# Kernel tuning notes

Hardware: AMD Instinct MI355X
Metric: run time of the kernel (lower is better)

The kernel has to match this reference:

```python
import jax, jax.numpy as jnp
import numpy as np

NUM_HEADS = 16

def _stablemax3_s(x):
    # 3rd-order Taylor approx of exp(x), Eq 38
    pos = 1.0 + x * (1.0 + 0.5 * x * (1.0 + x / 3.0))
    neg = 1.0 / (1.0 - x * (1.0 - 0.5 * x * (1.0 - x / 3.0)))
    return jnp.where(x >= 0, pos, neg)

def stablemax3(logits, axis=-1):
    logits = logits - jnp.max(logits, axis=axis, keepdims=True)
    s = _stablemax3_s(logits)
    return s / jnp.sum(s, axis=axis, keepdims=True)

def setup_inputs() -> dict:
    key = jax.random.key(0)
    k1, k2, k3 = jax.random.split(key, 3)
    B, S, D = 2, 2048, 1024
    x = jax.random.normal(k1, (B, S, D), dtype=jnp.float32)
    w_qkv = jax.random.normal(k2, (3 * D, D), dtype=jnp.float32) * 0.02
    w_out = jax.random.normal(k3, (D, D), dtype=jnp.float32) * 0.02
    b_out = jnp.zeros((D,), dtype=jnp.float32)
    return {"x": x, "w_qkv": w_qkv, "w_out": w_out, "b_out": b_out}

def reference(x, w_qkv, w_out, b_out):
    B, S, D = x.shape
    H = NUM_HEADS
    hd = D // H
    scale = hd ** (-0.5)
    qkv = x @ w_qkv.T                                  # [B, S, 3D]
    qkv = qkv.reshape(B, S, 3, H, hd)
    qkv = jnp.transpose(qkv, (2, 0, 3, 1, 4))          # [3, B, H, S, hd]
    q, k, v = qkv[0], qkv[1], qkv[2]                   # pos(.) is identity here
    attn = jnp.einsum('bhsd,bhtd->bhst', q, k) * scale # [B, H, S, S]
    attn = stablemax3(attn, axis=-1)
    out = jnp.einsum('bhst,bhtd->bhsd', attn, v)       # [B, H, S, hd]
    out = jnp.transpose(out, (0, 2, 1, 3)).reshape(B, S, D)
    return out @ w_out.T + b_out
```

## Files before the change

kernel.cpp:

```cpp
#include <hip/hip_runtime.h>

typedef _Float16 half8 __attribute__((ext_vector_type(8)));
typedef _Float16 half4 __attribute__((ext_vector_type(4)));
typedef _Float16 half2v __attribute__((ext_vector_type(2)));
typedef float floatx4 __attribute__((ext_vector_type(4)));
typedef unsigned int uint2v __attribute__((ext_vector_type(2)));
typedef unsigned int uint4v __attribute__((ext_vector_type(4)));

__device__ __forceinline__ void gl_lds16(const _Float16* g, _Float16* l) {
    __builtin_amdgcn_global_load_lds(
        (const __attribute__((address_space(1))) void*)g,
        (__attribute__((address_space(3))) void*)l, 16, 0, 0);
}

__device__ __forceinline__ half2v cvt_pk(float a, float b) {
    return __builtin_bit_cast(half2v, __builtin_amdgcn_cvt_pkrtz(a, b));
}

__device__ __forceinline__ half2v rcp2(half2v d) {
#if __has_builtin(__builtin_amdgcn_rcph)
    half2v r;
    r[0] = __builtin_amdgcn_rcph(d[0]);
    r[1] = __builtin_amdgcn_rcph(d[1]);
    return r;
#else
    half2v r;
    r[0] = (_Float16)__builtin_amdgcn_rcpf((float)d[0]);
    r[1] = (_Float16)__builtin_amdgcn_rcpf((float)d[1]);
    return r;
#endif
}

__device__ __forceinline__ float dot2acc(half2v a, float acc) {
#if __has_builtin(__builtin_amdgcn_fdot2)
    const half2v one = {(_Float16)1.0f, (_Float16)1.0f};
    return __builtin_amdgcn_fdot2(a, one, acc, false);
#else
    return acc + (float)a[0] + (float)a[1];
#endif
}

__device__ __forceinline__ half8 from4(half2v a, half2v b, half2v c, half2v d) {
    uint4v u = {__builtin_bit_cast(unsigned int, a), __builtin_bit_cast(unsigned int, b),
                __builtin_bit_cast(unsigned int, c), __builtin_bit_cast(unsigned int, d)};
    return __builtin_bit_cast(half8, u);
}

__device__ __forceinline__ half8 from_lohi(half4 lo, half4 hi) {
    uint2v l = __builtin_bit_cast(uint2v, lo);
    uint2v h = __builtin_bit_cast(uint2v, hi);
    uint4v u = {l[0], l[1], h[0], h[1]};
    return __builtin_bit_cast(half8, u);
}

__global__ __launch_bounds__(256) void cvt_xw(const floatx4* __restrict__ x,
                                              const floatx4* __restrict__ wq,
                                              half4* __restrict__ xh,
                                              half4* __restrict__ wqh) {
    int i = blockIdx.x * 256 + threadIdx.x;
    floatx4 v;
    half4 h;
    if (i < 1048576) {
        v = x[i];
#pragma unroll
        for (int j = 0; j < 4; ++j) h[j] = (_Float16)v[j];
        xh[i] = h;
    } else {
        int j4 = i - 1048576;
        v = wq[j4];
#pragma unroll
        for (int j = 0; j < 4; ++j) h[j] = (_Float16)v[j];
        wqh[j4] = h;
    }
}

__global__ __launch_bounds__(256) void cvt_f32_f16(const floatx4* __restrict__ in,
                                                   half4* __restrict__ out, int n4) {
    int i = blockIdx.x * 256 + threadIdx.x;
    if (i >= n4) return;
    floatx4 v = in[i];
    half4 h;
#pragma unroll
    for (int j = 0; j < 4; ++j) h[j] = (_Float16)v[j];
    out[i] = h;
}

__global__ __launch_bounds__(256) void gemm_qkv(const _Float16* __restrict__ A,
                                                const _Float16* __restrict__ B,
                                                _Float16* __restrict__ qh,
                                                _Float16* __restrict__ kh,
                                                _Float16* __restrict__ vth) {
    const int K = 1024;
    __shared__ _Float16 SH[128 * 68];
    _Float16* As = SH;
    _Float16* Bs = SH + 4096;
    const int t = threadIdx.x;
    const int lane = t & 63, w = t >> 6;
    const int l15 = lane & 15, quad = lane >> 4;
    const int wm = w >> 1, wn = w & 1;
    const int m0 = blockIdx.y * 128, n0 = blockIdx.x * 128;

    floatx4 acc[4][4];
    const floatx4 zf = {0.f, 0.f, 0.f, 0.f};
#pragma unroll
    for (int i = 0; i < 4; ++i)
#pragma unroll
        for (int j = 0; j < 4; ++j) acc[i][j] = zf;

    for (int kt = 0; kt < K; kt += 32) {
        __syncthreads();
#pragma unroll
        for (int it = 0; it < 2; ++it) {
            int cc = it * 256 + t;
            int row = cc >> 2, kc = cc & 3;
            gl_lds16(&A[(size_t)(m0 + row) * K + kt + kc * 8], &As[cc * 8]);
            gl_lds16(&B[(size_t)(n0 + row) * K + kt + kc * 8], &Bs[cc * 8]);
        }
        __syncthreads();
        half8 af[4], bfr[4];
#pragma unroll
        for (int i = 0; i < 4; ++i)
            af[i] = *(const half8*)&As[(wm * 64 + i * 16 + l15) * 32 + quad * 8];
#pragma unroll
        for (int i = 0; i < 4; ++i)
            bfr[i] = *(const half8*)&Bs[(wn * 64 + i * 16 + l15) * 32 + quad * 8];
#pragma unroll
        for (int mi = 0; mi < 4; ++mi)
#pragma unroll
            for (int ni = 0; ni < 4; ++ni)
                acc[mi][ni] = __builtin_amdgcn_mfma_f32_16x16x32_f16(af[mi], bfr[ni],
                                                                     acc[mi][ni], 0, 0, 0);
    }

    const int b = m0 >> 11, s0 = m0 & 2047;
#pragma unroll
    for (int hf = 0; hf < 2; ++hf) {
        __syncthreads();
        if (wn == hf) {
#pragma unroll
            for (int mi = 0; mi < 4; ++mi)
#pragma unroll
                for (int ni = 0; ni < 4; ++ni)
#pragma unroll
                    for (int r = 0; r < 4; ++r)
                        SH[(wm * 64 + mi * 16 + quad * 4 + r) * 68 + ni * 16 + l15] =
                            (_Float16)acc[mi][ni][r];
        }
        __syncthreads();
        const int cbase = n0 + hf * 64;
        if (n0 < 2048) {
            const int hh = (cbase & 1023) >> 6;
            _Float16* dst = (n0 < 1024 ? qh : kh) + (size_t)((b << 4) | hh) * 131072;
#pragma unroll
            for (int it = 0; it < 4; ++it) {
                int cc = it * 256 + t;
                int r = cc >> 3, c8 = cc & 7;
                half4 lo = *(const half4*)&SH[r * 68 + c8 * 8];
                half4 hi = *(const half4*)&SH[r * 68 + c8 * 8 + 4];
                *(half8*)&dst[(size_t)(s0 + r) * 64 + c8 * 8] = from_lohi(lo, hi);
            }
        } else {
            const int hh = (cbase - 2048) >> 6;
            _Float16* dst = vth + (size_t)((b << 4) | hh) * 131072;
#pragma unroll
            for (int it = 0; it < 4; ++it) {
                int cc = it * 256 + t;
                int d = cc >> 4, s8 = cc & 15;
                int sq = s8 & 7;
                int base = (s8 >> 3) * 64 + (sq >> 2) * 32 + (sq & 3) * 4;
                half8 v;
#pragma unroll
                for (int j = 0; j < 8; ++j)
                    v[j] = SH[(base + (j >> 2) * 16 + (j & 3)) * 68 + d];
                *(half8*)&dst[(size_t)d * 2048 + s0 + s8 * 8] = v;
            }
        }
    }
}

__global__ __launch_bounds__(256) void gemm_out(const _Float16* __restrict__ A,
                                                const _Float16* __restrict__ B,
                                                float* __restrict__ C,
                                                const float* __restrict__ bias) {
    const int K = 1024, N = 1024;
    __shared__ _Float16 SH[6144];
    _Float16* As = SH;
    _Float16* Bs = SH + 2048;
    const int t = threadIdx.x;
    const int lane = t & 63, w = t >> 6;
    const int l15 = lane & 15, quad = lane >> 4;
    const int wm = w >> 1, wn = w & 1;
    const int m0 = blockIdx.y * 64, n0 = blockIdx.x * 128;

    floatx4 acc[2][4];
    const floatx4 zf = {0.f, 0.f, 0.f, 0.f};
#pragma unroll
    for (int i = 0; i < 2; ++i)
#pragma unroll
        for (int j = 0; j < 4; ++j) acc[i][j] = zf;

    for (int kt = 0; kt < K; kt += 32) {
        __syncthreads();
        {
            int row = t >> 2, kc = t & 3;
            gl_lds16(&A[(size_t)(m0 + row) * K + kt + kc * 8], &As[t * 8]);
        }
#pragma unroll
        for (int it = 0; it < 2; ++it) {
            int cc = it * 256 + t;
            int row = cc >> 2, kc = cc & 3;
            gl_lds16(&B[(size_t)(n0 + row) * K + kt + kc * 8], &Bs[cc * 8]);
        }
        __syncthreads();
        half8 af[2], bfr[4];
#pragma unroll
        for (int i = 0; i < 2; ++i)
            af[i] = *(const half8*)&As[(wm * 32 + i * 16 + l15) * 32 + quad * 8];
#pragma unroll
        for (int i = 0; i < 4; ++i)
            bfr[i] = *(const half8*)&Bs[(wn * 64 + i * 16 + l15) * 32 + quad * 8];
#pragma unroll
        for (int mi = 0; mi < 2; ++mi)
#pragma unroll
            for (int ni = 0; ni < 4; ++ni)
                acc[mi][ni] = __builtin_amdgcn_mfma_f32_16x16x32_f16(af[mi], bfr[ni],
                                                                     acc[mi][ni], 0, 0, 0);
    }

#pragma unroll
    for (int mi = 0; mi < 2; ++mi) {
#pragma unroll
        for (int ni = 0; ni < 4; ++ni) {
            int col = n0 + wn * 64 + ni * 16 + l15;
            float bv = bias[col];
#pragma unroll
            for (int r = 0; r < 4; ++r) {
                int row = m0 + wm * 32 + mi * 16 + quad * 4 + r;
                C[(size_t)row * N + col] = acc[mi][ni][r] + bv;
            }
        }
    }
}

__global__ __launch_bounds__(256, 4) void attn_kernel(const _Float16* __restrict__ qh,
                                                      const _Float16* __restrict__ kh,
                                                      const _Float16* __restrict__ vth,
                                                      _Float16* __restrict__ out) {
    __shared__ _Float16 SM[16384];

    const int t = threadIdx.x;
    const int lane = t & 63, w = t >> 6;
    const int l15 = lane & 15, quad = lane >> 4;
    const int sw = l15 & 7;
    const int qg = w >> 1, kg = w & 1;
    const int bh = blockIdx.x;
    const int q0 = blockIdx.y * 64;
    const int b = bh >> 4, h = bh & 15;

    const _Float16* Qp = qh + (size_t)bh * 131072 + q0 * 64;
    const _Float16* Kp = kh + (size_t)bh * 131072;
    const _Float16* VTp = vth + (size_t)bh * 131072;

    const int row0 = t >> 3, cg0 = (t & 7) ^ (row0 & 7);
    const _Float16* K0 = &Kp[(size_t)row0 * 64 + cg0 * 8];
    const _Float16* V0 = &VTp[(size_t)row0 * 2048 + cg0 * 8];

    const floatx4 zf = {0.f, 0.f, 0.f, 0.f};

    half8 qf[2][2];
#pragma unroll
    for (int nh = 0; nh < 2; ++nh)
#pragma unroll
        for (int kk = 0; kk < 2; ++kk) {
            half8 q = *(const half8*)&Qp[(qg * 32 + nh * 16 + l15) * 64 + kk * 32 + quad * 8];
#pragma unroll
            for (int j = 0; j < 8; ++j) q[j] = q[j] * (_Float16)0.125f;
            qf[nh][kk] = q;
        }

    float rmax[2] = {-1.0e30f, -1.0e30f};
#pragma unroll
    for (int s = 0; s < 4; ++s)
        gl_lds16(K0 + s * 2048, &SM[s * 2048 + t * 8]);
    __syncthreads();
    {
        const _Float16* sKp = K0 + 8192;
        for (int i = 0, cur = 0; i < 16; ++i, cur ^= 1) {
            if (i < 15) {
                _Float16* kd = cur ? &SM[0] : &SM[8192];
#pragma unroll
                for (int s = 0; s < 4; ++s)
                    gl_lds16(sKp + s * 2048, kd + s * 2048 + t * 8);
                sKp += 8192;
            }
            const _Float16* Ks = cur ? &SM[8192] : &SM[0];
            half8 kf0[4], kf1[4];
#pragma unroll
            for (int Ti = 0; Ti < 4; ++Ti) {
                const int rb = ((kg * 4 + Ti) * 16 + l15) << 6;
                kf0[Ti] = *(const half8*)&Ks[rb + ((quad ^ sw) << 3)];
                kf1[Ti] = *(const half8*)&Ks[rb + (((4 + quad) ^ sw) << 3)];
            }
            floatx4 sa[4][2];
            __builtin_amdgcn_s_setprio(1);
#pragma unroll
            for (int Ti = 0; Ti < 4; ++Ti)
#pragma unroll
                for (int nh = 0; nh < 2; ++nh)
                    sa[Ti][nh] = __builtin_amdgcn_mfma_f32_16x16x32_f16(kf0[Ti], qf[nh][0],
                                                                        zf, 0, 0, 0);
#pragma unroll
            for (int Ti = 0; Ti < 4; ++Ti)
#pragma unroll
                for (int nh = 0; nh < 2; ++nh)
                    sa[Ti][nh] = __builtin_amdgcn_mfma_f32_16x16x32_f16(kf1[Ti], qf[nh][1],
                                                                        sa[Ti][nh], 0, 0, 0);
            __builtin_amdgcn_s_setprio(0);
#pragma unroll
            for (int Ti = 0; Ti < 4; ++Ti)
#pragma unroll
                for (int nh = 0; nh < 2; ++nh)
#pragma unroll
                    for (int r = 0; r < 4; ++r)
                        rmax[nh] = fmaxf(rmax[nh], sa[Ti][nh][r]);
            __syncthreads();
        }
    }
#pragma unroll
    for (int nh = 0; nh < 2; ++nh) {
        rmax[nh] = fmaxf(rmax[nh], __shfl_xor(rmax[nh], 16, 64));
        rmax[nh] = fmaxf(rmax[nh], __shfl_xor(rmax[nh], 32, 64));
    }
    {
        float* EXM = (float*)SM;
        if (quad == 0) {
#pragma unroll
            for (int nh = 0; nh < 2; ++nh)
                EXM[((qg * 2 + nh) * 2 + kg) * 16 + l15] = rmax[nh];
        }
        __syncthreads();
#pragma unroll
        for (int nh = 0; nh < 2; ++nh)
            rmax[nh] = fmaxf(EXM[((qg * 2 + nh) * 2 + 0) * 16 + l15],
                             EXM[((qg * 2 + nh) * 2 + 1) * 16 + l15]);
        __syncthreads();
    }
    const floatx4 xmv[2] = {{-rmax[0], -rmax[0], -rmax[0], -rmax[0]},
                            {-rmax[1], -rmax[1], -rmax[1], -rmax[1]}};

    const half2v cA = {(_Float16)(-1.0f / 6.0f), (_Float16)(-1.0f / 6.0f)};
    const half2v cB = {(_Float16)0.5f, (_Float16)0.5f};
    const half2v cC = {(_Float16)-1.0f, (_Float16)-1.0f};
    const half2v cD = {(_Float16)1.0f, (_Float16)1.0f};

    float rsum[2] = {0.f, 0.f};
    floatx4 oacc[4][2];
#pragma unroll
    for (int i = 0; i < 4; ++i) { oacc[i][0] = zf; oacc[i][1] = zf; }

    auto tile_step = [&](const _Float16* Ks, const _Float16* VTs) {
        half8 kf0[2], kf1[2];
#pragma unroll
        for (int Ti = 0; Ti < 2; ++Ti) {
            const int rb = ((kg * 2 + Ti) * 16 + l15) << 6;
            kf0[Ti] = *(const half8*)&Ks[rb + ((quad ^ sw) << 3)];
            kf1[Ti] = *(const half8*)&Ks[rb + (((4 + quad) ^ sw) << 3)];
        }
        floatx4 sa[2][2];
        __builtin_amdgcn_s_setprio(1);
#pragma unroll
        for (int Ti = 0; Ti < 2; ++Ti)
#pragma unroll
            for (int nh = 0; nh < 2; ++nh)
                sa[Ti][nh] = __builtin_amdgcn_mfma_f32_16x16x32_f16(kf0[Ti], qf[nh][0],
                                                                    xmv[nh], 0, 0, 0);
#pragma unroll
        for (int Ti = 0; Ti < 2; ++Ti)
#pragma unroll
            for (int nh = 0; nh < 2; ++nh)
                sa[Ti][nh] = __builtin_amdgcn_mfma_f32_16x16x32_f16(kf1[Ti], qf[nh][1],
                                                                    sa[Ti][nh], 0, 0, 0);
        __builtin_amdgcn_s_setprio(0);
        half8 vf[4];
#pragma unroll
        for (int di = 0; di < 4; ++di)
            vf[di] = *(const half8*)&VTs[((di * 16 + l15) << 6) +
                                         ((((kg << 2) + quad) ^ sw) << 3)];
#pragma unroll
        for (int nh = 0; nh < 2; ++nh) {
            half2v p2m[4];
#pragma unroll
            for (int m = 0; m < 4; ++m) {
                int Ti = m >> 1;
                int r0 = (m & 1) * 2;
                half2v x2 = cvt_pk(sa[Ti][nh][r0], sa[Ti][nh][r0 + 1]);
                half2v hp = __builtin_elementwise_fma(x2, cA, cB);
                hp = __builtin_elementwise_fma(x2, hp, cC);
                hp = __builtin_elementwise_fma(x2, hp, cD);
                half2v p2 = rcp2(hp);
                rsum[nh] = dot2acc(p2, rsum[nh]);
                p2m[m] = p2;
            }
            half8 pb = from4(p2m[0], p2m[1], p2m[2], p2m[3]);
            __builtin_amdgcn_s_setprio(1);
#pragma unroll
            for (int di = 0; di < 4; ++di)
                oacc[di][nh] = __builtin_amdgcn_mfma_f32_16x16x32_f16(vf[di], pb,
                                                                      oacc[di][nh], 0, 0, 0);
            __builtin_amdgcn_s_setprio(0);
        }
    };

    gl_lds16(K0, &SM[t * 8]);
    gl_lds16(K0 + 2048, &SM[2048 + t * 8]);
    gl_lds16(V0, &SM[8192 + t * 8]);
    gl_lds16(V0 + 65536, &SM[8192 + 2048 + t * 8]);
    __syncthreads();

    {
        const _Float16* sK = K0 + 4096;
        const _Float16* sV = V0 + 64;
        for (int i = 0; i < 16; ++i) {
            gl_lds16(sK, &SM[4096 + t * 8]);
            gl_lds16(sK + 2048, &SM[4096 + 2048 + t * 8]);
            gl_lds16(sV, &SM[12288 + t * 8]);
            gl_lds16(sV + 65536, &SM[12288 + 2048 + t * 8]);
            sK += 4096; sV += 64;
            tile_step(&SM[0], &SM[8192]);
            __syncthreads();
            if (i < 15) {
                gl_lds16(sK, &SM[t * 8]);
                gl_lds16(sK + 2048, &SM[2048 + t * 8]);
                gl_lds16(sV, &SM[8192 + t * 8]);
                gl_lds16(sV + 65536, &SM[8192 + 2048 + t * 8]);
                sK += 4096; sV += 64;
            }
            tile_step(&SM[4096], &SM[12288]);
            __syncthreads();
        }
    }

#pragma unroll
    for (int nh = 0; nh < 2; ++nh) {
        rsum[nh] += __shfl_xor(rsum[nh], 16, 64);
        rsum[nh] += __shfl_xor(rsum[nh], 32, 64);
    }

    float* EXO = (float*)SM;
    float* EXS = (float*)(SM + 8192);
    _Float16* Os = SM + 8320;
    if (kg) {
#pragma unroll
        for (int nh = 0; nh < 2; ++nh)
#pragma unroll
            for (int di = 0; di < 4; ++di)
                *(floatx4*)&EXO[(((((qg * 2 + nh) * 4 + di) * 4 + quad) * 16) + l15) * 4] =
                    oacc[di][nh];
        if (quad == 0) {
#pragma unroll
            for (int nh = 0; nh < 2; ++nh)
                EXS[(qg * 2 + nh) * 16 + l15] = rsum[nh];
        }
    }
    __syncthreads();
    if (!kg) {
        float inv[2];
#pragma unroll
        for (int nh = 0; nh < 2; ++nh)
            inv[nh] = 1.0f / (rsum[nh] + EXS[(qg * 2 + nh) * 16 + l15]);
#pragma unroll
        for (int nh = 0; nh < 2; ++nh)
#pragma unroll
            for (int di = 0; di < 4; ++di) {
                floatx4 part = *(const floatx4*)
                    &EXO[(((((qg * 2 + nh) * 4 + di) * 4 + quad) * 16) + l15) * 4];
                half4 hv;
#pragma unroll
                for (int r = 0; r < 4; ++r)
                    hv[r] = (_Float16)((oacc[di][nh][r] + part[r]) * inv[nh]);
                *(half4*)&Os[(qg * 32 + nh * 16 + l15) * 72 + di * 16 + quad * 4] = hv;
            }
    }
    __syncthreads();
    _Float16* Op = out + (size_t)(b * 2048 + q0) * 1024 + h * 64;
#pragma unroll
    for (int it = 0; it < 2; ++it) {
        int cc = it * 256 + t;
        int r = cc >> 3, c8 = cc & 7;
        *(half8*)&Op[(size_t)r * 1024 + c8 * 8] = *(const half8*)&Os[r * 72 + c8 * 8];
    }
}

extern "C" void kernel_launch(void* const* d_in, const int* in_sizes, int n_in,
                              void* d_out, int out_size, void* d_ws, size_t ws_size,
                              hipStream_t stream) {
    const float* x_f = (const float*)d_in[0];
    const float* wqkv_f = (const float*)d_in[1];
    const float* wout_f = (const float*)d_in[2];
    const float* bias_f = (const float*)d_in[3];

    char* ws = (char*)d_ws;
    _Float16* xh = (_Float16*)(ws);
    _Float16* aoh = xh;
    _Float16* wqh = (_Float16*)(ws + 8388608);
    _Float16* woh = wqh;
    _Float16* qh = (_Float16*)(ws + 14680064);
    _Float16* kh = (_Float16*)(ws + 23068672);
    _Float16* vth = (_Float16*)(ws + 31457280);

    cvt_xw<<<7168, 256, 0, stream>>>((const floatx4*)x_f, (const floatx4*)wqkv_f,
                                     (half4*)xh, (half4*)wqh);
    gemm_qkv<<<dim3(24, 32), 256, 0, stream>>>(xh, wqh, qh, kh, vth);
    cvt_f32_f16<<<1024, 256, 0, stream>>>((const floatx4*)wout_f, (half4*)woh, 262144);
    attn_kernel<<<dim3(32, 32), 256, 0, stream>>>(qh, kh, vth, aoh);
    gemm_out<<<dim3(8, 64), 256, 0, stream>>>(aoh, woh, (float*)d_out, bias_f);
}
```

Before: 204.1 us.

## Double-buffer LDS tiles in QKV and output projection GEMMs

Both projection GEMMs now use two LDS buffers. The global-to-LDS load of the next K tile is issued before the MFMA work on the current tile, so the loop needs one barrier per tile instead of two. The aim is to hide global load latency behind compute and cut barrier stalls. The cost is double the LDS per block, which may lower occupancy, plus a main loop unrolled by two.

```diff
diff --git a/kernel.cpp b/kernel.cpp
--- a/kernel.cpp
+++ b/kernel.cpp
@@ -91,9 +91,11 @@
                                                 _Float16* __restrict__ kh,
                                                 _Float16* __restrict__ vth) {
     const int K = 1024;
-    __shared__ _Float16 SH[128 * 68];
-    _Float16* As = SH;
-    _Float16* Bs = SH + 4096;
+    __shared__ _Float16 SH[16384];
+    _Float16* As0 = SH;
+    _Float16* Bs0 = SH + 4096;
+    _Float16* As1 = SH + 8192;
+    _Float16* Bs1 = SH + 12288;
     const int t = threadIdx.x;
     const int lane = t & 63, w = t >> 6;
     const int l15 = lane & 15, quad = lane >> 4;
@@ -107,16 +109,17 @@
 #pragma unroll
         for (int j = 0; j < 4; ++j) acc[i][j] = zf;
 
-    for (int kt = 0; kt < K; kt += 32) {
-        __syncthreads();
-#pragma unroll
-        for (int it = 0; it < 2; ++it) {
-            int cc = it * 256 + t;
-            int row = cc >> 2, kc = cc & 3;
-            gl_lds16(&A[(size_t)(m0 + row) * K + kt + kc * 8], &As[cc * 8]);
-            gl_lds16(&B[(size_t)(n0 + row) * K + kt + kc * 8], &Bs[cc * 8]);
-        }
-        __syncthreads();
+    const _Float16* Asrc = &A[(size_t)(m0 + (t >> 2)) * K + (t & 3) * 8];
+    const _Float16* Bsrc = &B[(size_t)(n0 + (t >> 2)) * K + (t & 3) * 8];
+    const size_t r64 = (size_t)64 * K;
+
+    auto stage = [&](int kt, _Float16* As, _Float16* Bs) {
+        gl_lds16(Asrc + kt, &As[t * 8]);
+        gl_lds16(Asrc + r64 + kt, &As[2048 + t * 8]);
+        gl_lds16(Bsrc + kt, &Bs[t * 8]);
+        gl_lds16(Bsrc + r64 + kt, &Bs[2048 + t * 8]);
+    };
+    auto compute = [&](const _Float16* As, const _Float16* Bs) {
         half8 af[4], bfr[4];
 #pragma unroll
         for (int i = 0; i < 4; ++i)
@@ -130,6 +133,17 @@
             for (int ni = 0; ni < 4; ++ni)
                 acc[mi][ni] = __builtin_amdgcn_mfma_f32_16x16x32_f16(af[mi], bfr[ni],
                                                                      acc[mi][ni], 0, 0, 0);
+    };
+
+    stage(0, As0, Bs0);
+    __syncthreads();
+    for (int kt = 0; kt < K; kt += 64) {
+        stage(kt + 32, As1, Bs1);
+        compute(As0, Bs0);
+        __syncthreads();
+        if (kt + 64 < K) stage(kt + 64, As0, Bs0);
+        compute(As1, Bs1);
+        __syncthreads();
     }
 
     const int b = m0 >> 11, s0 = m0 & 2047;
@@ -183,9 +197,11 @@
                                                 float* __restrict__ C,
                                                 const float* __restrict__ bias) {
     const int K = 1024, N = 1024;
-    __shared__ _Float16 SH[6144];
-    _Float16* As = SH;
-    _Float16* Bs = SH + 2048;
+    __shared__ _Float16 SH[12288];
+    _Float16* As0 = SH;
+    _Float16* Bs0 = SH + 2048;
+    _Float16* As1 = SH + 6144;
+    _Float16* Bs1 = SH + 8192;
     const int t = threadIdx.x;
     const int lane = t & 63, w = t >> 6;
     const int l15 = lane & 15, quad = lane >> 4;
@@ -199,19 +215,16 @@
 #pragma unroll
         for (int j = 0; j < 4; ++j) acc[i][j] = zf;
 
-    for (int kt = 0; kt < K; kt += 32) {
-        __syncthreads();
-        {
-            int row = t >> 2, kc = t & 3;
-            gl_lds16(&A[(size_t)(m0 + row) * K + kt + kc * 8], &As[t * 8]);
-        }
-#pragma unroll
-        for (int it = 0; it < 2; ++it) {
-            int cc = it * 256 + t;
-            int row = cc >> 2, kc = cc & 3;
-            gl_lds16(&B[(size_t)(n0 + row) * K + kt + kc * 8], &Bs[cc * 8]);
-        }
-        __syncthreads();
+    const _Float16* Asrc = &A[(size_t)(m0 + (t >> 2)) * K + (t & 3) * 8];
+    const _Float16* Bsrc = &B[(size_t)(n0 + (t >> 2)) * K + (t & 3) * 8];
+    const size_t r64 = (size_t)64 * K;
+
+    auto stage = [&](int kt, _Float16* As, _Float16* Bs) {
+        gl_lds16(Asrc + kt, &As[t * 8]);
+        gl_lds16(Bsrc + kt, &Bs[t * 8]);
+        gl_lds16(Bsrc + r64 + kt, &Bs[2048 + t * 8]);
+    };
+    auto compute = [&](const _Float16* As, const _Float16* Bs) {
         half8 af[2], bfr[4];
 #pragma unroll
         for (int i = 0; i < 2; ++i)
@@ -225,6 +238,17 @@
             for (int ni = 0; ni < 4; ++ni)
                 acc[mi][ni] = __builtin_amdgcn_mfma_f32_16x16x32_f16(af[mi], bfr[ni],
                                                                      acc[mi][ni], 0, 0, 0);
+    };
+
+    stage(0, As0, Bs0);
+    __syncthreads();
+    for (int kt = 0; kt < K; kt += 64) {
+        stage(kt + 32, As1, Bs1);
+        compute(As0, Bs0);
+        __syncthreads();
+        if (kt + 64 < K) stage(kt + 64, As0, Bs0);
+        compute(As1, Bs1);
+        __syncthreads();
     }
 
 #pragma unroll
```

Measured after the change: 205.0 us. No clear change (+0.4%).
